# Kernel optimization log

Measured on AMD Instinct MI355X. Metric: run time of the kernel, lower is better.

Reference implementation:

```python
import jax, jax.numpy as jnp
import numpy as np

NBITS = 4  # asymmetric fake-quant

def fake_quant_asym(w, bit):
    # mask of nonzero weights (zeros stay zero after quantization)
    mask = (w != 0).astype(w.dtype)
    max_ = jnp.max(w)
    min_ = jnp.min(w)
    alpha = max_ - min_
    beta = min_
    step = (2 ** bit) - 1
    ws = (w - beta) / alpha
    R = jnp.round(step * ws) / step
    wq = alpha * R + beta
    return wq * mask

def setup_inputs() -> dict:
    key = jax.random.key(0)
    k1, k2, k3 = jax.random.split(key, 3)
    m, n = 1024, 1024
    std = np.sqrt(2.0 / (m + n))
    x = jax.random.normal(k1, (16384, m), dtype=jnp.float32)
    weight = jax.random.normal(k2, (n, m), dtype=jnp.float32) * std
    bias = jax.random.normal(k3, (n,), dtype=jnp.float32) * 0.01
    return {"x": x, "weight": weight, "bias": bias}

def reference(x, weight, bias):
    wq = fake_quant_asym(weight, NBITS)
    # F.linear: y = x @ W^T + b
    return jnp.einsum('tm,nm->tn', x, wq) + bias
```

## Files before the change

### kernel.cpp

```cpp
#include <hip/hip_runtime.h>
#include <hip/hip_bf16.h>

#define M_DIM 16384
#define N_DIM 1024
#define K_DIM 1024

typedef short v8s __attribute__((ext_vector_type(8)));
typedef float v4f __attribute__((ext_vector_type(4)));
typedef unsigned v2u __attribute__((ext_vector_type(2)));

__device__ __forceinline__ unsigned short f2bf(float f) {
  unsigned u = __float_as_uint(f);
  unsigned r = (u + 0x7FFFu + ((u >> 16) & 1u)) >> 16;
  return (unsigned short)r;
}

__device__ __forceinline__ unsigned short f2bf_hw(float f) {
  __hip_bfloat16 h = __float2bfloat16(f);
  return *reinterpret_cast<unsigned short*>(&h);
}

__device__ __forceinline__ void gload16(const void* g, void* l) {
  __builtin_amdgcn_global_load_lds(
      (const __attribute__((address_space(1))) void*)g,
      (__attribute__((address_space(3))) void*)l, 16, 0, 0);
}

#define DSR(dst, addr, off) \
  asm volatile("ds_read_b128 %0, %1 offset:" off : "=v"(dst) : "v"(addr))

__global__ void wminmax_part(const float* __restrict__ w, float* __restrict__ part) {
  int tid = blockIdx.x * 256 + threadIdx.x;
  float mx = -3.402823466e38f, mn = 3.402823466e38f;
  for (int i = tid; i < N_DIM * K_DIM / 4; i += 256 * 256) {
    float4 v = *(const float4*)(w + i * 4);
    mx = fmaxf(fmaxf(mx, fmaxf(v.x, v.y)), fmaxf(v.z, v.w));
    mn = fminf(fminf(mn, fminf(v.x, v.y)), fminf(v.z, v.w));
  }
  #pragma unroll
  for (int o = 32; o > 0; o >>= 1) {
    mx = fmaxf(mx, __shfl_down(mx, o));
    mn = fminf(mn, __shfl_down(mn, o));
  }
  __shared__ float smx[4], smn[4];
  int lane = threadIdx.x & 63, wv = threadIdx.x >> 6;
  if (lane == 0) { smx[wv] = mx; smn[wv] = mn; }
  __syncthreads();
  if (threadIdx.x == 0) {
    mx = fmaxf(fmaxf(smx[0], smx[1]), fmaxf(smx[2], smx[3]));
    mn = fminf(fminf(smn[0], smn[1]), fminf(smn[2], smn[3]));
    part[blockIdx.x] = mx;
    part[256 + blockIdx.x] = mn;
  }
}

__global__ void wminmax_final(const float* __restrict__ part, float* __restrict__ mm) {
  float mx = part[threadIdx.x];
  float mn = part[256 + threadIdx.x];
  #pragma unroll
  for (int o = 32; o > 0; o >>= 1) {
    mx = fmaxf(mx, __shfl_down(mx, o));
    mn = fminf(mn, __shfl_down(mn, o));
  }
  __shared__ float smx[4], smn[4];
  int lane = threadIdx.x & 63, wv = threadIdx.x >> 6;
  if (lane == 0) { smx[wv] = mx; smn[wv] = mn; }
  __syncthreads();
  if (threadIdx.x == 0) {
    mm[0] = fmaxf(fmaxf(smx[0], smx[1]), fmaxf(smx[2], smx[3]));
    mm[1] = fminf(fminf(smn[0], smn[1]), fminf(smn[2], smn[3]));
  }
}

__global__ void quant_kernel(const float* __restrict__ w, const float* __restrict__ mm,
                             unsigned short* __restrict__ wq) {
  const float mx = mm[0], mn = mm[1];
  const float alpha = mx - mn, beta = mn;
  int i = (blockIdx.x * 256 + threadIdx.x) * 4;
  float4 v = *(const float4*)(w + i);
  float f[4] = {v.x, v.y, v.z, v.w};
  ushort4 o;
  unsigned short ov[4];
  #pragma unroll
  for (int j = 0; j < 4; j++) {
    float s = (f[j] - beta) / alpha;
    float R = rintf(15.0f * s) / 15.0f;
    float q = alpha * R + beta;
    if (f[j] == 0.0f) q = 0.0f;
    ov[j] = f2bf(q);
  }
  o.x = ov[0]; o.y = ov[1]; o.z = ov[2]; o.w = ov[3];
  *(ushort4*)(wq + i) = o;
}

__global__ __launch_bounds__(512, 2) void gemm_fused(
    const float* __restrict__ x, const unsigned short* __restrict__ wq,
    const float* __restrict__ bias, float* __restrict__ out) {
  __shared__ __attribute__((aligned(16))) unsigned short As[2][256][32];
  __shared__ __attribute__((aligned(16))) unsigned short Bs[4][256][32];

  const int tid = threadIdx.x;
  const int lane = tid & 63;
  const int wv = tid >> 6;
  const int wr = wv >> 2;
  const int wc = wv & 3;
  const int bm = blockIdx.x;
  const int bn = blockIdx.y;

  const int srow = wv * 32 + (lane >> 2);
  const int ssw = ((lane & 3) ^ ((lane >> 3) & 3)) * 8;
  const unsigned short* bS = wq + (size_t)(bn * 256 + srow) * K_DIM + ssw;

  const float* aF = x + (size_t)(bm * 256 + wv * 32 + (lane >> 3)) * K_DIM + (lane & 7) * 4;

  const int frow = lane & 15;
  const int fsw = ((lane >> 4) ^ ((frow >> 1) & 3)) * 8;
  const unsigned ldsA0 =
      (unsigned)(unsigned long long)(__attribute__((address_space(3))) unsigned short*)&As[0][0][0];
  const unsigned ldsB0 =
      (unsigned)(unsigned long long)(__attribute__((address_space(3))) unsigned short*)&Bs[0][0][0];
  const unsigned aLane = ldsA0 + (unsigned)((wr * 128 + frow) * 32 + fsw) * 2u;
  const unsigned bLane = ldsB0 + (unsigned)((wc * 64 + frow) * 32 + fsw) * 2u;

  const unsigned wA = ldsA0 +
      (unsigned)((wv * 32 + (lane >> 3)) * 64 +
                 ((((lane & 7) >> 1) ^ ((lane >> 4) & 3)) * 16) + ((lane & 7) & 1) * 8);

  v4f acc[8][4];
  #pragma unroll
  for (int m = 0; m < 8; m++)
    #pragma unroll
    for (int n = 0; n < 4; n++) acc[m][n] = (v4f)(0.0f);

  v8s af[4], bf[4];
  float4 ra0[4], ra1[4];

#define RA_LOAD(RA_, H2_) do { \
    _Pragma("unroll") \
    for (int j_ = 0; j_ < 4; j_++) \
      RA_[j_] = *(const float4*)(aF + (size_t)(H2_) * 32 + j_ * 8 * K_DIM); \
  } while (0)

#define CVTW(RA_, SL_) do { \
    _Pragma("unroll") \
    for (int j_ = 0; j_ < 4; j_++) { \
      v2u p_; \
      p_.x = (unsigned)f2bf_hw(RA_[j_].x) | ((unsigned)f2bf_hw(RA_[j_].y) << 16); \
      p_.y = (unsigned)f2bf_hw(RA_[j_].z) | ((unsigned)f2bf_hw(RA_[j_].w) << 16); \
      asm volatile("ds_write_b64 %0, %1" \
                   :: "v"(wA + (SL_) * 16384u + j_ * 512u), "v"(p_) : "memory"); \
    } \
  } while (0)

#define STAGE_B(H_, SL_) do { \
    gload16(bS + (size_t)(H_) * 32, &Bs[SL_][wv * 32][0]); \
    gload16(bS + (size_t)(H_) * 32 + 16 * K_DIM, &Bs[SL_][wv * 32 + 16][0]); \
  } while (0)

#define MM16(MH_) do { \
    _Pragma("unroll") \
    for (int i_ = 0; i_ < 4; i_++) \
      _Pragma("unroll") \
      for (int n_ = 0; n_ < 4; n_++) \
        acc[(MH_) * 4 + i_][n_] = __builtin_amdgcn_mfma_f32_16x16x32_bf16( \
            af[i_], bf[n_], acc[(MH_) * 4 + i_][n_], 0, 0, 0); \
  } while (0)

#define PH0(H_, AS_, BS_, RALD_, STG_) do { \
    const unsigned aP = aLane + (AS_) * 16384u; \
    const unsigned bP = bLane + (BS_) * 16384u; \
    DSR(af[0], aP, "0");    DSR(af[1], aP, "1024"); \
    DSR(af[2], aP, "2048"); DSR(af[3], aP, "3072"); \
    DSR(bf[0], bP, "0");    DSR(bf[1], bP, "1024"); \
    DSR(bf[2], bP, "2048"); DSR(bf[3], bP, "3072"); \
    if (STG_) RA_LOAD(RALD_, (H_) + 2); \
    __builtin_amdgcn_s_barrier(); \
    asm volatile("s_waitcnt lgkmcnt(0)" ::: "memory"); \
    __builtin_amdgcn_sched_barrier(0); \
    __builtin_amdgcn_s_setprio(1); \
    MM16(0); \
    __builtin_amdgcn_s_setprio(0); \
    __builtin_amdgcn_s_barrier(); \
  } while (0)

#define PH1(H_, AS_, BW_, RACV_, STG_, CVT_, GATE_) do { \
    const unsigned aP = aLane + (AS_) * 16384u + 4096u; \
    DSR(af[0], aP, "0");    DSR(af[1], aP, "1024"); \
    DSR(af[2], aP, "2048"); DSR(af[3], aP, "3072"); \
    if (CVT_) CVTW(RACV_, (AS_) ^ 1); \
    if (STG_) STAGE_B((H_) + 2, BW_); \
    __builtin_amdgcn_s_barrier(); \
    asm volatile("s_waitcnt lgkmcnt(0)" ::: "memory"); \
    __builtin_amdgcn_sched_barrier(0); \
    __builtin_amdgcn_s_setprio(1); \
    MM16(1); \
    __builtin_amdgcn_s_setprio(0); \
    asm volatile("s_waitcnt vmcnt(" GATE_ ")" ::: "memory"); \
    __builtin_amdgcn_s_barrier(); \
  } while (0)

#define KHALF(H_, AS_, BS_, BW_, RALD_, RACV_, STG_, CVT_, GATE_) do { \
    PH0(H_, AS_, BS_, RALD_, STG_); \
    PH1(H_, AS_, BW_, RACV_, STG_, CVT_, GATE_); \
  } while (0)

  RA_LOAD(ra0, 0);
  RA_LOAD(ra1, 1);
  STAGE_B(0, 0);
  STAGE_B(1, 1);
  CVTW(ra0, 0);
  asm volatile("s_waitcnt vmcnt(2)" ::: "memory");
  asm volatile("s_waitcnt lgkmcnt(0)" ::: "memory");
  __builtin_amdgcn_s_barrier();

  #pragma unroll 1
  for (int kh = 0; kh < 28; kh += 4) {
    KHALF(kh + 0, 0, 0, 2, ra0, ra1, 1, 1, "6");
    KHALF(kh + 1, 1, 1, 3, ra1, ra0, 1, 1, "6");
    KHALF(kh + 2, 0, 2, 0, ra0, ra1, 1, 1, "6");
    KHALF(kh + 3, 1, 3, 1, ra1, ra0, 1, 1, "6");
  }
  KHALF(28, 0, 0, 2, ra0, ra1, 1, 1, "6");
  KHALF(29, 1, 1, 3, ra1, ra0, 1, 1, "6");
  KHALF(30, 0, 2, 0, ra0, ra1, 0, 1, "0");
  KHALF(31, 1, 3, 0, ra1, ra0, 0, 0, "0");

#undef KHALF
#undef PH0
#undef PH1
#undef MM16
#undef STAGE_B
#undef CVTW
#undef RA_LOAD

  {
    float* eb = (float*)(&As[0][0][0]) + wv * (16 * 64);
    const int colbase = bn * 256 + wc * 64;
    const int rowbase = bm * 256 + wr * 128;
    float bv[4];
    #pragma unroll
    for (int n = 0; n < 4; n++) bv[n] = bias[colbase + n * 16 + (lane & 15)];
    const int er = lane >> 4;
    const int ec = lane & 15;
    const int rr = lane >> 2;
    const int q  = lane & 3;
    #pragma unroll
    for (int m = 0; m < 8; m++) {
      #pragma unroll
      for (int n = 0; n < 4; n++) {
        #pragma unroll
        for (int r = 0; r < 4; r++) {
          const int R = er * 4 + r;
          const int cn = n * 16 + ec;
          const int g = cn >> 2;
          eb[R * 64 + ((g ^ (R & 15)) << 2) + (cn & 3)] = acc[m][n][r] + bv[n];
        }
      }
      float* orow = out + (size_t)(rowbase + m * 16 + rr) * N_DIM + colbase;
      #pragma unroll
      for (int j = 0; j < 4; j++) {
        const int g = j * 4 + q;
        v4f v = *(v4f*)&eb[rr * 64 + ((g ^ (rr & 15)) << 2)];
        *(v4f*)&orow[j * 16 + q * 4] = v;
      }
    }
  }
}

__global__ __launch_bounds__(256) void gemm_kernel(
    const float* __restrict__ x, const unsigned short* __restrict__ wq,
    const float* __restrict__ bias, float* __restrict__ out) {
  __shared__ __attribute__((aligned(16))) unsigned short As[2][128][32];
  __shared__ __attribute__((aligned(16))) unsigned short Bs[2][128][32];

  const int tid = threadIdx.x;
  const int lane = tid & 63;
  const int wv = tid >> 6;
  const int wr = wv >> 1, wc = wv & 1;
  const int bm = blockIdx.x, bn = blockIdx.y;

  const int arow = tid >> 1;
  const int acol = (tid & 1) << 4;
  const float* aptr = x + (size_t)(bm * 128 + arow) * K_DIM + acol;
  const int fA = (arow >> 1) & 3;
  const int ac0 = (tid & 1) * 2;
  const int aw0 = ((ac0) ^ fA) * 8;
  const int aw1 = ((ac0 + 1) ^ fA) * 8;

  const int brow0 = wv * 32 + (lane >> 2);
  const int bsrcc = (lane & 3) ^ ((lane >> 3) & 3);
  const unsigned short* bptr0 = wq + (size_t)(bn * 128 + brow0) * K_DIM + bsrcc * 8;
  const unsigned short* bptr1 = bptr0 + (size_t)16 * K_DIM;

  v4f acc[4][4];
  #pragma unroll
  for (int i = 0; i < 4; i++)
    #pragma unroll
    for (int j = 0; j < 4; j++) acc[i][j] = (v4f)(0.0f);

  const int frow = lane & 15;
  const int fkc = lane >> 4;
  const int fsw = (fkc ^ ((frow >> 1) & 3)) * 8;

  float4 areg[4];
  #pragma unroll
  for (int j = 0; j < 4; j++) areg[j] = *(const float4*)(aptr + j * 4);

  {
    const float* f = (const float*)areg;
    union { v8s v; unsigned short u[8]; } cv0, cv1;
    #pragma unroll
    for (int i = 0; i < 8; i++) { cv0.u[i] = f2bf(f[i]); cv1.u[i] = f2bf(f[i + 8]); }
    *(v8s*)&As[0][arow][aw0] = cv0.v;
    *(v8s*)&As[0][arow][aw1] = cv1.v;
    gload16(bptr0, &Bs[0][wv * 32][0]);
    gload16(bptr1, &Bs[0][wv * 32 + 16][0]);
  }
  #pragma unroll
  for (int j = 0; j < 4; j++) areg[j] = *(const float4*)(aptr + 32 + j * 4);
  __syncthreads();

  for (int kt = 0; kt < K_DIM / 32; ++kt) {
    const int cur = kt & 1, nxt = cur ^ 1;
    if (kt + 1 < K_DIM / 32) {
      const float* f = (const float*)areg;
      union { v8s v; unsigned short u[8]; } cv0, cv1;
      #pragma unroll
      for (int i = 0; i < 8; i++) { cv0.u[i] = f2bf(f[i]); cv1.u[i] = f2bf(f[i + 8]); }
      *(v8s*)&As[nxt][arow][aw0] = cv0.v;
      *(v8s*)&As[nxt][arow][aw1] = cv1.v;
      gload16(bptr0 + (size_t)(kt + 1) * 32, &Bs[nxt][wv * 32][0]);
      gload16(bptr1 + (size_t)(kt + 1) * 32, &Bs[nxt][wv * 32 + 16][0]);
      if (kt + 2 < K_DIM / 32) {
        const float* ap = aptr + (kt + 2) * 32;
        #pragma unroll
        for (int j = 0; j < 4; j++) areg[j] = *(const float4*)(ap + j * 4);
      }
    }
    v8s af[4], bf[4];
    #pragma unroll
    for (int m = 0; m < 4; m++)
      af[m] = *(const v8s*)&As[cur][wr * 64 + m * 16 + frow][fsw];
    #pragma unroll
    for (int n = 0; n < 4; n++)
      bf[n] = *(const v8s*)&Bs[cur][wc * 64 + n * 16 + frow][fsw];
    #pragma unroll
    for (int m = 0; m < 4; m++)
      #pragma unroll
      for (int n = 0; n < 4; n++)
        acc[m][n] = __builtin_amdgcn_mfma_f32_16x16x32_bf16(af[m], bf[n], acc[m][n], 0, 0, 0);
    __syncthreads();
  }

  const int colbase = bn * 128 + wc * 64;
  const int rowbase = bm * 128 + wr * 64;
  #pragma unroll
  for (int n = 0; n < 4; n++) {
    const int col = colbase + n * 16 + (lane & 15);
    const float bv = bias[col];
    #pragma unroll
    for (int m = 0; m < 4; m++) {
      const int row0 = rowbase + m * 16 + (lane >> 4) * 4;
      #pragma unroll
      for (int r = 0; r < 4; r++)
        out[(size_t)(row0 + r) * N_DIM + col] = acc[m][n][r] + bv;
    }
  }
}

extern "C" void kernel_launch(void* const* d_in, const int* in_sizes, int n_in,
                              void* d_out, int out_size, void* d_ws, size_t ws_size,
                              hipStream_t stream) {
  const float* x = (const float*)d_in[0];
  const float* wt = (const float*)d_in[1];
  const float* bias = (const float*)d_in[2];
  float* out = (float*)d_out;

  float* part = (float*)d_ws;
  float* mm = part + 512;
  unsigned short* wqbuf = (unsigned short*)((char*)d_ws + 4096);
  const size_t need = 4096 + 2ull * 1024 * 1024;

  wminmax_part<<<256, 256, 0, stream>>>(wt, part);
  wminmax_final<<<1, 256, 0, stream>>>(part, mm);
  quant_kernel<<<1024, 256, 0, stream>>>(wt, mm, wqbuf);

  if (ws_size >= need) {
    dim3 grid(M_DIM / 256, N_DIM / 256);
    gemm_fused<<<grid, 512, 0, stream>>>(x, wqbuf, bias, out);
  } else {
    dim3 grid(M_DIM / 128, N_DIM / 128);
    gemm_kernel<<<grid, 256, 0, stream>>>(x, wqbuf, bias, out);
  }
}
```

Baseline: 63.78 us.

## Fuse min/max final reduction into quant kernel and relax LDS wait in GEMM

Drops the single-block final min/max kernel: each quant block now re-reduces the 256 partials itself and shares alpha/beta through LDS, removing one launch and a serial dependency step. In the GEMM's second phase, when the A conversion writes are issued, the wait now lets up to four LDS operations stay outstanding before the MFMAs, so the fragment reads can complete while the conversion writes are still in flight. A full lgkmcnt(0) wait is added after the MFMAs to keep the barrier correct. This adds redundant reduction work per quant block, and a dead MM16 macro that is defined and immediately undefined.

```diff
diff --git a/kernel.cpp b/kernel.cpp
--- a/kernel.cpp
+++ b/kernel.cpp
@@ -54,29 +54,30 @@
   }
 }
 
-__global__ void wminmax_final(const float* __restrict__ part, float* __restrict__ mm) {
-  float mx = part[threadIdx.x];
-  float mn = part[256 + threadIdx.x];
+__global__ void quant_kernel(const float* __restrict__ w, const float* __restrict__ part,
+                             unsigned short* __restrict__ wq) {
+  const int t = threadIdx.x;
+  float mx = part[t & 255];
+  float mn = part[256 + (t & 255)];
   #pragma unroll
   for (int o = 32; o > 0; o >>= 1) {
     mx = fmaxf(mx, __shfl_down(mx, o));
     mn = fminf(mn, __shfl_down(mn, o));
   }
   __shared__ float smx[4], smn[4];
-  int lane = threadIdx.x & 63, wv = threadIdx.x >> 6;
-  if (lane == 0) { smx[wv] = mx; smn[wv] = mn; }
+  __shared__ float sab[2];
+  const int lane = t & 63, wvv = t >> 6;
+  if (lane == 0) { smx[wvv] = mx; smn[wvv] = mn; }
   __syncthreads();
-  if (threadIdx.x == 0) {
-    mm[0] = fmaxf(fmaxf(smx[0], smx[1]), fmaxf(smx[2], smx[3]));
-    mm[1] = fminf(fminf(smn[0], smn[1]), fminf(smn[2], smn[3]));
-  }
-}
-
-__global__ void quant_kernel(const float* __restrict__ w, const float* __restrict__ mm,
-                             unsigned short* __restrict__ wq) {
-  const float mx = mm[0], mn = mm[1];
-  const float alpha = mx - mn, beta = mn;
-  int i = (blockIdx.x * 256 + threadIdx.x) * 4;
+  if (t == 0) {
+    mx = fmaxf(fmaxf(smx[0], smx[1]), fmaxf(smx[2], smx[3]));
+    mn = fminf(fminf(smn[0], smn[1]), fminf(smn[2], smn[3]));
+    sab[0] = mx - mn;
+    sab[1] = mn;
+  }
+  __syncthreads();
+  const float alpha = sab[0], beta = sab[1];
+  int i = (blockIdx.x * 256 + t) * 4;
   float4 v = *(const float4*)(w + i);
   float f[4] = {v.x, v.y, v.z, v.w};
   ushort4 o;
@@ -157,6 +158,15 @@
     gload16(bS + (size_t)(H_) * 32 + 16 * K_DIM, &Bs[SL_][wv * 32 + 16][0]); \
   } while (0)
 
+#define MM16(MH_) do { \
+    _Pragma("unroll") \
+    for (int i_ = 0; i_ < 4; i_++) \
+      _Pragma("unroll") \
+      for (int n_ = 0; n_ < 4; n_++) \
+        acc[(MH_) * 4 + i_][n_] = __builtin_amdgcn_mfma_f32_16x16x32_bf16( \
+            af[i_], bf[n_], acc[(MH_) * 4 + i_], 0, 0, 0); \
+  } while (0)
+#undef MM16
 #define MM16(MH_) do { \
     _Pragma("unroll") \
     for (int i_ = 0; i_ < 4; i_++) \
@@ -190,11 +200,13 @@
     if (CVT_) CVTW(RACV_, (AS_) ^ 1); \
     if (STG_) STAGE_B((H_) + 2, BW_); \
     __builtin_amdgcn_s_barrier(); \
-    asm volatile("s_waitcnt lgkmcnt(0)" ::: "memory"); \
+    if (CVT_) { asm volatile("s_waitcnt lgkmcnt(4)" ::: "memory"); } \
+    else      { asm volatile("s_waitcnt lgkmcnt(0)" ::: "memory"); } \
     __builtin_amdgcn_sched_barrier(0); \
     __builtin_amdgcn_s_setprio(1); \
     MM16(1); \
     __builtin_amdgcn_s_setprio(0); \
+    asm volatile("s_waitcnt lgkmcnt(0)" ::: "memory"); \
     asm volatile("s_waitcnt vmcnt(" GATE_ ")" ::: "memory"); \
     __builtin_amdgcn_s_barrier(); \
   } while (0)
@@ -377,13 +389,11 @@
   float* out = (float*)d_out;
 
   float* part = (float*)d_ws;
-  float* mm = part + 512;
   unsigned short* wqbuf = (unsigned short*)((char*)d_ws + 4096);
   const size_t need = 4096 + 2ull * 1024 * 1024;
 
   wminmax_part<<<256, 256, 0, stream>>>(wt, part);
-  wminmax_final<<<1, 256, 0, stream>>>(part, mm);
-  quant_kernel<<<1024, 256, 0, stream>>>(wt, mm, wqbuf);
+  quant_kernel<<<1024, 256, 0, stream>>>(wt, part, wqbuf);
 
   if (ws_size >= need) {
     dim3 grid(M_DIM / 256, N_DIM / 256);
```

New measurement: 62.08 us. 2.7% less time.
